# Kernel tuning notes

Hardware: AMD Instinct MI355X
Metric: run time of the kernel (lower is better)

Reference implementation:

```python
import jax, jax.numpy as jnp
import numpy as np

INPUT_SIZE = 1024  # enc_dim + dec_dim after concat
ENC_DIM = 512
DEC_DIM = 512
INNER_DIM = 512
VOCAB = 2048


def setup_inputs() -> dict:
    key = jax.random.key(0)
    k1, k2, k3, k4, k5, k6 = jax.random.split(key, 6)
    B, T, U = 4, 256, 128
    enc_state = jax.random.normal(k1, (B, T, ENC_DIM), dtype=jnp.float32)
    dec_state = jax.random.normal(k2, (B, U, DEC_DIM), dtype=jnp.float32)
    # forward_layer: Linear(input_size, inner_dim); stored as [in, out] for jax
    s1 = 1.0 / np.sqrt(INPUT_SIZE)
    W1 = jax.random.uniform(k3, (INPUT_SIZE, INNER_DIM), jnp.float32, -s1, s1)
    b1 = jax.random.uniform(k4, (INNER_DIM,), jnp.float32, -s1, s1)
    s2 = 1.0 / np.sqrt(INNER_DIM)
    W2 = jax.random.uniform(k5, (INNER_DIM, VOCAB), jnp.float32, -s2, s2)
    b2 = jax.random.uniform(k6, (VOCAB,), jnp.float32, -s2, s2)
    return {"enc_state": enc_state, "dec_state": dec_state,
            "W1": W1, "b1": b1, "W2": W2, "b2": b2}


def reference(enc_state, dec_state, W1, b1, W2, b2):
    # JointNet: concat(enc_repeat, dec_repeat) @ W1 + b1 -> tanh -> @ W2 + b2.
    # Since W1 acts on the concat axis, split it: concat @ W1 == enc @ W1_e + dec @ W1_d
    # (mathematically identical, avoids materializing the [B,T,U,2D] concat tensor).
    W1_enc = W1[:ENC_DIM]   # [D_enc, inner]
    W1_dec = W1[ENC_DIM:]   # [D_dec, inner]
    enc_proj = jnp.einsum('btd,dh->bth', enc_state, W1_enc)  # [B,T,H]
    dec_proj = jnp.einsum('bud,dh->buh', dec_state, W1_dec)  # [B,U,H]
    h = jnp.tanh(enc_proj[:, :, None, :] + dec_proj[:, None, :, :] + b1)  # [B,T,U,H]
    logits = jnp.einsum('btuh,hv->btuv', h, W2) + b2  # [B,T,U,V]
    return logits
```

## Files before the change

### kernel.cpp

```cpp
#include <hip/hip_runtime.h>
#include <hip/hip_bf16.h>


typedef __attribute__((ext_vector_type(4))) float f32x4;
typedef __attribute__((ext_vector_type(8))) __bf16 bf16x8;
typedef __attribute__((ext_vector_type(8))) unsigned short u16x8;

__device__ __forceinline__ float bf2f(unsigned short u) {
  unsigned int x = ((unsigned int)u) << 16;
  return __builtin_bit_cast(float, x);
}
__device__ __forceinline__ unsigned short f2bf(float f) {
  unsigned int x = __builtin_bit_cast(unsigned int, f);
  x += 0x7fff + ((x >> 16) & 1);
  return (unsigned short)(x >> 16);
}
__device__ __forceinline__ float tanh_fast(float x) {
  float e = __expf(2.0f * x);
  return 1.0f - 2.0f * __builtin_amdgcn_rcpf(e + 1.0f);
}

typedef __attribute__((address_space(3))) unsigned int lds_u32;
typedef const __attribute__((address_space(1))) unsigned int glb_u32;
__device__ __forceinline__ void gl16(const void* g, void* l) {
  __builtin_amdgcn_global_load_lds((glb_u32*)g, (lds_u32*)l, 16, 0, 0);
}

#define BAR __builtin_amdgcn_s_barrier()
#define LGKM0 asm volatile("s_waitcnt lgkmcnt(0)" ::: "memory")
#define VMCNT(n) asm volatile("s_waitcnt vmcnt(" #n ")" ::: "memory")
#define MEMPIN asm volatile("" ::: "memory")

__global__ __launch_bounds__(512) void proj8_kernel(
    const float* __restrict__ enc, const float* __restrict__ dec,
    const float* __restrict__ W1, const float* __restrict__ b1,
    float* __restrict__ enc_proj, unsigned short* __restrict__ decb) {
  __shared__ float xs[8][512];
  const int bid = blockIdx.x;
  const bool isenc = bid < 128;
  const int rows0 = (isenc ? bid : bid - 128) * 8;
  const float* src = (isenc ? enc : dec) + (size_t)rows0 * 512;
  const int tid = threadIdx.x;
#pragma unroll
  for (int j = 0; j < 2; ++j) {
    int v = j * 512 + tid;
    int row = v >> 7;
    int c4 = (v & 127) << 2;
    *(f32x4*)&xs[row][c4] = *(const f32x4*)&src[(size_t)row * 512 + c4];
  }
  __syncthreads();
  const int h = tid;
  const float* wp = W1 + (isenc ? 0 : (size_t)512 * 512) + h;
  float acc[8];
  float init = isenc ? 0.f : b1[h];
#pragma unroll
  for (int r = 0; r < 8; ++r) acc[r] = init;
#pragma unroll 4
  for (int k = 0; k < 512; ++k) {
    float wv = wp[(size_t)k * 512];
#pragma unroll
    for (int r = 0; r < 8; ++r) acc[r] = fmaf(xs[r][k], wv, acc[r]);
  }
  if (isenc) {
#pragma unroll
    for (int r = 0; r < 8; ++r) enc_proj[(size_t)(rows0 + r) * 512 + h] = acc[r];
  } else {
#pragma unroll
    for (int r = 0; r < 8; ++r) decb[(size_t)(rows0 + r) * 512 + h] = f2bf(acc[r]);
  }
}

__global__ __launch_bounds__(256) void w2t_kernel(const float* __restrict__ W2,
                                                  unsigned short* __restrict__ W2t) {
  __shared__ unsigned short tile[32][33];
  int bn = blockIdx.x;
  int bk = blockIdx.y;
  int tx = threadIdx.x & 31;
  int ty = threadIdx.x >> 5;
#pragma unroll
  for (int i = 0; i < 32; i += 8)
    tile[ty + i][tx] = f2bf(W2[(size_t)(bk * 32 + ty + i) * 2048 + bn * 32 + tx]);
  __syncthreads();
#pragma unroll
  for (int i = 0; i < 32; i += 8)
    W2t[(size_t)(bn * 32 + ty + i) * 512 + bk * 32 + tx] = tile[tx][ty + i];
}

__global__ __launch_bounds__(256) void h_kernel(
    const float* __restrict__ encp, const unsigned short* __restrict__ decb,
    unsigned short* __restrict__ Hout) {
  int gid = blockIdx.x * 256 + threadIdx.x;
  int m = gid >> 6;
  int hc = (gid & 63) << 3;
  int bt = m >> 7;
  int bu = ((m >> 15) << 7) | (m & 127);
  u16x8 dv = *(const u16x8*)(decb + (size_t)bu * 512 + hc);
  f32x4 e0 = *(const f32x4*)(encp + (size_t)bt * 512 + hc);
  f32x4 e1 = *(const f32x4*)(encp + (size_t)bt * 512 + hc + 4);
  u16x8 hv;
#pragma unroll
  for (int j = 0; j < 4; ++j) hv[j] = f2bf(tanh_fast(bf2f(dv[j]) + e0[j]));
#pragma unroll
  for (int j = 0; j < 4; ++j) hv[4 + j] = f2bf(tanh_fast(bf2f(dv[4 + j]) + e1[j]));
  *(u16x8*)(Hout + (size_t)m * 512 + hc) = hv;
}

__device__ __forceinline__ void stage_half(const char* src, char* dst_region,
                                           int half, int w, int lane) {
#pragma unroll
  for (int r = 0; r < 2; ++r) {
    int dbase = half * 16384 + r * 8192 + w * 1024;
    int d = dbase + lane * 16;
    int s = d ^ (((d >> 9) & 1) << 5);
    gl16(src + (size_t)(s >> 7) * 1024 + (s & 127), dst_region + dbase);
  }
}

__device__ __forceinline__ void load_a(const char* Ar, int a_base, int MH,
                                       bf16x8 (&afr)[4][2]) {
#pragma unroll
  for (int mi = 0; mi < 4; ++mi)
#pragma unroll
    for (int kk = 0; kk < 2; ++kk)
      afr[mi][kk] = *(const bf16x8*)(Ar + a_base + MH * 8192 + mi * 2048 + kk * 64);
}
__device__ __forceinline__ void load_b(const char* Br, int b_base, int NH,
                                       bf16x8 (&bh)[2][2]) {
#pragma unroll
  for (int ni = 0; ni < 2; ++ni)
#pragma unroll
    for (int kk = 0; kk < 2; ++kk)
      bh[ni][kk] = *(const bf16x8*)(Br + b_base + NH * 4096 + ni * 2048 + kk * 64);
}

template <int MH, int NH>
__device__ __forceinline__ void mfma_quad(bf16x8 (&afr)[4][2], bf16x8 (&bh)[2][2],
                                          f32x4 (&acc)[8][4]) {
  __builtin_amdgcn_s_setprio(1);
#pragma unroll
  for (int mi = 0; mi < 4; ++mi)
#pragma unroll
    for (int ni = 0; ni < 2; ++ni)
#pragma unroll
      for (int kk = 0; kk < 2; ++kk)
        acc[MH * 4 + mi][NH * 2 + ni] = __builtin_amdgcn_mfma_f32_16x16x32_bf16(
            afr[mi][kk], bh[ni][kk], acc[MH * 4 + mi][NH * 2 + ni], 0, 0, 0);
  __builtin_amdgcn_s_setprio(0);
}

__global__ __launch_bounds__(512, 2) void gemm8_kernel(
    const unsigned short* __restrict__ H,
    const unsigned short* __restrict__ W2t,
    const float* __restrict__ b2,
    float* __restrict__ out) {
  __shared__ __align__(1024) char smem[131072];
  char* A0 = smem;
  char* B0 = smem + 32768;
  char* A1 = smem + 65536;
  char* B1 = smem + 98304;

  const int bid = blockIdx.x;
  const int wg = (bid & 7) * 512 + (bid >> 3);
  const int my = wg >> 3;
  const int ny = wg & 7;

  const int tid = threadIdx.x;
  const int lane = tid & 63;
  const int w = tid >> 6;
  const int wm = w >> 2;
  const int wn = w & 3;
  const int fr = lane & 15;
  const int fq = lane >> 4;
  const int xr = (fr & 4) ? 32 : 0;

  const char* ha = (const char*)(H + (size_t)my * 256 * 512);
  const char* wb = (const char*)(W2t + (size_t)ny * 256 * 512);

  const int a_base = (wm * 128 + fr) * 128 + ((fq * 16) ^ xr);
  const int b_base = (wn * 64 + fr) * 128 + ((fq * 16) ^ xr);

  f32x4 acc[8][4];
#pragma unroll
  for (int i = 0; i < 8; ++i)
#pragma unroll
    for (int j = 0; j < 4; ++j) acc[i][j] = (f32x4){0.f, 0.f, 0.f, 0.f};
  bf16x8 afr[4][2];
  bf16x8 bfr[2][2][2];

  stage_half(ha, A0, 0, w, lane);        stage_half(ha, A0, 1, w, lane);
  stage_half(wb, B0, 0, w, lane);        stage_half(wb, B0, 1, w, lane);
  stage_half(ha + 128, A1, 0, w, lane);  stage_half(ha + 128, A1, 1, w, lane);
  stage_half(wb + 128, B1, 0, w, lane);  stage_half(wb + 128, B1, 1, w, lane);
  VMCNT(0);
  BAR; MEMPIN;

  for (int i = 0; i < 4; ++i) {
    const int t = 2 * i;
    const char* sA1 = ha + (size_t)(t + 1) * 128;
    const char* sA2 = ha + (size_t)(t + 2) * 128;
    const char* sB2 = wb + (size_t)(t + 2) * 128;
    const char* sB3 = wb + (size_t)(t + 3) * 128;
    const bool si = (i >= 1);
    const bool so = (i <= 2);

    load_a(A0, a_base, 0, afr);
    load_b(B0, b_base, 0, bfr[0]);
    if (si) stage_half(sA1, A1, 0, w, lane);
    BAR; LGKM0;
    mfma_quad<0, 0>(afr, bfr[0], acc);
    BAR; MEMPIN;

    load_b(B0, b_base, 1, bfr[1]);
    if (si) stage_half(sA1, A1, 1, w, lane);
    BAR; LGKM0;
    mfma_quad<0, 1>(afr, bfr[1], acc);
    BAR; MEMPIN;

    load_a(A0, a_base, 1, afr);
    if (so) stage_half(sB2, B0, 0, w, lane);
    BAR; LGKM0;
    mfma_quad<1, 0>(afr, bfr[0], acc);
    BAR; MEMPIN;

    if (so) {
      stage_half(sB2, B0, 1, w, lane);
      stage_half(sA2, A0, 0, w, lane);
      stage_half(sA2, A0, 1, w, lane);
    }
    BAR; LGKM0;
    mfma_quad<1, 1>(afr, bfr[1], acc);
    if (i < 3) { VMCNT(8); } else { VMCNT(0); }
    BAR; MEMPIN;

    load_a(A1, a_base, 0, afr);
    load_b(B1, b_base, 0, bfr[0]);
    BAR; LGKM0;
    mfma_quad<0, 0>(afr, bfr[0], acc);
    BAR; MEMPIN;

    load_b(B1, b_base, 1, bfr[1]);
    BAR; LGKM0;
    mfma_quad<0, 1>(afr, bfr[1], acc);
    BAR; MEMPIN;

    load_a(A1, a_base, 1, afr);
    if (so) stage_half(sB3, B1, 0, w, lane);
    BAR; LGKM0;
    mfma_quad<1, 0>(afr, bfr[0], acc);
    BAR; MEMPIN;

    if (so) stage_half(sB3, B1, 1, w, lane);
    BAR; LGKM0;
    mfma_quad<1, 1>(afr, bfr[1], acc);
    if (i < 3) { VMCNT(4); } else { VMCNT(0); }
    BAR; MEMPIN;
  }

  float* lslice = (float*)(smem + w * 4352);
  const size_t orow0 = (size_t)my * 256 + wm * 128;
  const int ncol0 = ny * 256 + wn * 64;
  float bv[4];
#pragma unroll
  for (int ni4 = 0; ni4 < 4; ++ni4) bv[ni4] = b2[ncol0 + ni4 * 16 + fr];

  const int rrow = lane >> 4;
  const int rcol = (lane & 15) * 4;
#pragma unroll
  for (int mi8 = 0; mi8 < 8; ++mi8) {
#pragma unroll
    for (int ni4 = 0; ni4 < 4; ++ni4)
#pragma unroll
      for (int r = 0; r < 4; ++r)
        lslice[(fq * 4 + r) * 68 + ni4 * 16 + fr] = acc[mi8][ni4][r] + bv[ni4];
#pragma unroll
    for (int j = 0; j < 4; ++j) {
      int row = j * 4 + rrow;
      f32x4 v = *(const f32x4*)&lslice[row * 68 + rcol];
      __builtin_nontemporal_store(
          v, (f32x4*)&out[(orow0 + mi8 * 16 + row) * 2048 + ncol0 + rcol]);
    }
  }
}

extern "C" void kernel_launch(void* const* d_in, const int* in_sizes, int n_in,
                              void* d_out, int out_size, void* d_ws, size_t ws_size,
                              hipStream_t stream) {
  const float* enc = (const float*)d_in[0];
  const float* dec = (const float*)d_in[1];
  const float* W1  = (const float*)d_in[2];
  const float* b1  = (const float*)d_in[3];
  const float* W2  = (const float*)d_in[4];
  const float* b2  = (const float*)d_in[5];
  float* out = (float*)d_out;

  char* ws = (char*)d_ws;
  float* enc_proj = (float*)ws;
  unsigned short* decb = (unsigned short*)(ws + (2u << 20));
  unsigned short* W2t  = (unsigned short*)(ws + (2u << 20) + (512u << 10));
  unsigned short* Hbuf = (unsigned short*)(ws + (8u << 20));

  proj8_kernel<<<192, 512, 0, stream>>>(enc, dec, W1, b1, enc_proj, decb);
  w2t_kernel<<<dim3(64, 16), 256, 0, stream>>>(W2, W2t);
  h_kernel<<<32768, 256, 0, stream>>>(enc_proj, decb, Hbuf);
  gemm8_kernel<<<4096, 512, 0, stream>>>(Hbuf, W2t, b2, out);
}
```

Before: 427.0 us.

## Replace 256x256 GEMM tile with 256x128 tile and 3-stage K=32 pipeline

The main logits GEMM drops its 256x256 output tile, 8-wave 2x4 layout and 128KB double buffer. It now uses a 256x128 tile with a 4x2 wave layout and K steps of 32 through a 3-slot, 72KB LDS ring with XOR swizzle. This allows up to 4 blocks per CU and uses a simpler one-barrier-per-step schedule, aiming for higher occupancy and better latency hiding. In exchange, W2 tiles are reused less, H is re-read twice as often, and barriers are more frequent.

Result: faster. 406.1 us (-4.9%).

```diff
diff --git a/kernel.cpp b/kernel.cpp
--- a/kernel.cpp
+++ b/kernel.cpp
@@ -105,181 +105,114 @@
   *(u16x8*)(Hout + (size_t)m * 512 + hc) = hv;
 }
 
-__device__ __forceinline__ void stage_half(const char* src, char* dst_region,
-                                           int half, int w, int lane) {
-#pragma unroll
-  for (int r = 0; r < 2; ++r) {
-    int dbase = half * 16384 + r * 8192 + w * 1024;
-    int d = dbase + lane * 16;
-    int s = d ^ (((d >> 9) & 1) << 5);
-    gl16(src + (size_t)(s >> 7) * 1024 + (s & 127), dst_region + dbase);
-  }
-}
-
-__device__ __forceinline__ void load_a(const char* Ar, int a_base, int MH,
-                                       bf16x8 (&afr)[4][2]) {
-#pragma unroll
-  for (int mi = 0; mi < 4; ++mi)
-#pragma unroll
-    for (int kk = 0; kk < 2; ++kk)
-      afr[mi][kk] = *(const bf16x8*)(Ar + a_base + MH * 8192 + mi * 2048 + kk * 64);
-}
-__device__ __forceinline__ void load_b(const char* Br, int b_base, int NH,
-                                       bf16x8 (&bh)[2][2]) {
-#pragma unroll
-  for (int ni = 0; ni < 2; ++ni)
-#pragma unroll
-    for (int kk = 0; kk < 2; ++kk)
-      bh[ni][kk] = *(const bf16x8*)(Br + b_base + NH * 4096 + ni * 2048 + kk * 64);
-}
-
-template <int MH, int NH>
-__device__ __forceinline__ void mfma_quad(bf16x8 (&afr)[4][2], bf16x8 (&bh)[2][2],
-                                          f32x4 (&acc)[8][4]) {
-  __builtin_amdgcn_s_setprio(1);
-#pragma unroll
-  for (int mi = 0; mi < 4; ++mi)
-#pragma unroll
-    for (int ni = 0; ni < 2; ++ni)
-#pragma unroll
-      for (int kk = 0; kk < 2; ++kk)
-        acc[MH * 4 + mi][NH * 2 + ni] = __builtin_amdgcn_mfma_f32_16x16x32_bf16(
-            afr[mi][kk], bh[ni][kk], acc[MH * 4 + mi][NH * 2 + ni], 0, 0, 0);
-  __builtin_amdgcn_s_setprio(0);
-}
-
-__global__ __launch_bounds__(512, 2) void gemm8_kernel(
+
+__global__ __launch_bounds__(512, 4) void gemm32_kernel(
     const unsigned short* __restrict__ H,
     const unsigned short* __restrict__ W2t,
     const float* __restrict__ b2,
     float* __restrict__ out) {
-  __shared__ __align__(1024) char smem[131072];
-  char* A0 = smem;
-  char* B0 = smem + 32768;
-  char* A1 = smem + 65536;
-  char* B1 = smem + 98304;
+  __shared__ __align__(1024) char smem[73728];
 
   const int bid = blockIdx.x;
-  const int wg = (bid & 7) * 512 + (bid >> 3);
-  const int my = wg >> 3;
-  const int ny = wg & 7;
+  const int wg = (bid & 7) * 1024 + (bid >> 3);
+  const int my = wg >> 4;
+  const int ny = wg & 15;
 
   const int tid = threadIdx.x;
   const int lane = tid & 63;
   const int w = tid >> 6;
-  const int wm = w >> 2;
-  const int wn = w & 3;
+  const int wm = w >> 1;
+  const int wn = w & 1;
   const int fr = lane & 15;
   const int fq = lane >> 4;
-  const int xr = (fr & 4) ? 32 : 0;
 
   const char* ha = (const char*)(H + (size_t)my * 256 * 512);
-  const char* wb = (const char*)(W2t + (size_t)ny * 256 * 512);
-
-  const int a_base = (wm * 128 + fr) * 128 + ((fq * 16) ^ xr);
-  const int b_base = (wn * 64 + fr) * 128 + ((fq * 16) ^ xr);
-
-  f32x4 acc[8][4];
-#pragma unroll
-  for (int i = 0; i < 8; ++i)
+  const char* wb = (const char*)(W2t + (size_t)ny * 128 * 512);
+
+  size_t srcA[2], srcB;
+#pragma unroll
+  for (int p = 0; p < 2; ++p) {
+    int d = p * 8192 + w * 1024 + lane * 16;
+    int r = d >> 6;
+    int c = (d >> 4) & 3;
+    srcA[p] = (size_t)r * 1024 + (size_t)((c ^ (r & 3)) << 4);
+  }
+  {
+    int d = w * 1024 + lane * 16;
+    int r = d >> 6;
+    int c = (d >> 4) & 3;
+    srcB = (size_t)r * 1024 + (size_t)((c ^ (r & 3)) << 4);
+  }
+
+  const int swz = (fq ^ (fr & 3)) << 4;
+  const int ldsA = (wm * 64 + fr) * 64 + swz;
+  const int ldsB = 16384 + (wn * 64 + fr) * 64 + swz;
+
+  f32x4 acc[4][4];
+#pragma unroll
+  for (int i = 0; i < 4; ++i)
 #pragma unroll
     for (int j = 0; j < 4; ++j) acc[i][j] = (f32x4){0.f, 0.f, 0.f, 0.f};
-  bf16x8 afr[4][2];
-  bf16x8 bfr[2][2][2];
-
-  stage_half(ha, A0, 0, w, lane);        stage_half(ha, A0, 1, w, lane);
-  stage_half(wb, B0, 0, w, lane);        stage_half(wb, B0, 1, w, lane);
-  stage_half(ha + 128, A1, 0, w, lane);  stage_half(ha + 128, A1, 1, w, lane);
-  stage_half(wb + 128, B1, 0, w, lane);  stage_half(wb + 128, B1, 1, w, lane);
-  VMCNT(0);
+
+#define STAGE(tt, slot)                                         \
+  do {                                                          \
+    char* sl = smem + (slot)*24576;                             \
+    gl16(ha + srcA[0] + (tt)*64, sl + w * 1024);                \
+    gl16(ha + srcA[1] + (tt)*64, sl + 8192 + w * 1024);         \
+    gl16(wb + srcB + (tt)*64, sl + 16384 + w * 1024);           \
+  } while (0)
+
+  STAGE(0, 0);
+  STAGE(1, 1);
+
+#pragma unroll
+  for (int t = 0; t < 16; ++t) {
+    if (t < 15) { VMCNT(3); } else { VMCNT(0); }
+    BAR; MEMPIN;
+    const char* As = smem + (t % 3) * 24576;
+    bf16x8 a4[4], b4[4];
+#pragma unroll
+    for (int mi = 0; mi < 4; ++mi) a4[mi] = *(const bf16x8*)(As + ldsA + mi * 1024);
+#pragma unroll
+    for (int ni = 0; ni < 4; ++ni) b4[ni] = *(const bf16x8*)(As + ldsB + ni * 1024);
+    if (t + 2 < 16) STAGE(t + 2, (t + 2) % 3);
+    LGKM0;
+    __builtin_amdgcn_s_setprio(1);
+#pragma unroll
+    for (int mi = 0; mi < 4; ++mi)
+#pragma unroll
+      for (int ni = 0; ni < 4; ++ni)
+        acc[mi][ni] = __builtin_amdgcn_mfma_f32_16x16x32_bf16(
+            a4[mi], b4[ni], acc[mi][ni], 0, 0, 0);
+    __builtin_amdgcn_s_setprio(0);
+  }
   BAR; MEMPIN;
 
-  for (int i = 0; i < 4; ++i) {
-    const int t = 2 * i;
-    const char* sA1 = ha + (size_t)(t + 1) * 128;
-    const char* sA2 = ha + (size_t)(t + 2) * 128;
-    const char* sB2 = wb + (size_t)(t + 2) * 128;
-    const char* sB3 = wb + (size_t)(t + 3) * 128;
-    const bool si = (i >= 1);
-    const bool so = (i <= 2);
-
-    load_a(A0, a_base, 0, afr);
-    load_b(B0, b_base, 0, bfr[0]);
-    if (si) stage_half(sA1, A1, 0, w, lane);
-    BAR; LGKM0;
-    mfma_quad<0, 0>(afr, bfr[0], acc);
-    BAR; MEMPIN;
-
-    load_b(B0, b_base, 1, bfr[1]);
-    if (si) stage_half(sA1, A1, 1, w, lane);
-    BAR; LGKM0;
-    mfma_quad<0, 1>(afr, bfr[1], acc);
-    BAR; MEMPIN;
-
-    load_a(A0, a_base, 1, afr);
-    if (so) stage_half(sB2, B0, 0, w, lane);
-    BAR; LGKM0;
-    mfma_quad<1, 0>(afr, bfr[0], acc);
-    BAR; MEMPIN;
-
-    if (so) {
-      stage_half(sB2, B0, 1, w, lane);
-      stage_half(sA2, A0, 0, w, lane);
-      stage_half(sA2, A0, 1, w, lane);
-    }
-    BAR; LGKM0;
-    mfma_quad<1, 1>(afr, bfr[1], acc);
-    if (i < 3) { VMCNT(8); } else { VMCNT(0); }
-    BAR; MEMPIN;
-
-    load_a(A1, a_base, 0, afr);
-    load_b(B1, b_base, 0, bfr[0]);
-    BAR; LGKM0;
-    mfma_quad<0, 0>(afr, bfr[0], acc);
-    BAR; MEMPIN;
-
-    load_b(B1, b_base, 1, bfr[1]);
-    BAR; LGKM0;
-    mfma_quad<0, 1>(afr, bfr[1], acc);
-    BAR; MEMPIN;
-
-    load_a(A1, a_base, 1, afr);
-    if (so) stage_half(sB3, B1, 0, w, lane);
-    BAR; LGKM0;
-    mfma_quad<1, 0>(afr, bfr[0], acc);
-    BAR; MEMPIN;
-
-    if (so) stage_half(sB3, B1, 1, w, lane);
-    BAR; LGKM0;
-    mfma_quad<1, 1>(afr, bfr[1], acc);
-    if (i < 3) { VMCNT(4); } else { VMCNT(0); }
-    BAR; MEMPIN;
-  }
-
   float* lslice = (float*)(smem + w * 4352);
-  const size_t orow0 = (size_t)my * 256 + wm * 128;
-  const int ncol0 = ny * 256 + wn * 64;
+  const size_t orow0 = (size_t)my * 256 + wm * 64;
+  const int ncol0 = ny * 128 + wn * 64;
   float bv[4];
 #pragma unroll
-  for (int ni4 = 0; ni4 < 4; ++ni4) bv[ni4] = b2[ncol0 + ni4 * 16 + fr];
+  for (int ni = 0; ni < 4; ++ni) bv[ni] = b2[ncol0 + ni * 16 + fr];
 
   const int rrow = lane >> 4;
   const int rcol = (lane & 15) * 4;
 #pragma unroll
-  for (int mi8 = 0; mi8 < 8; ++mi8) {
-#pragma unroll
-    for (int ni4 = 0; ni4 < 4; ++ni4)
+  for (int mi = 0; mi < 4; ++mi) {
+#pragma unroll
+    for (int ni = 0; ni < 4; ++ni)
 #pragma unroll
       for (int r = 0; r < 4; ++r)
-        lslice[(fq * 4 + r) * 68 + ni4 * 16 + fr] = acc[mi8][ni4][r] + bv[ni4];
+        lslice[(fq * 4 + r) * 68 + ni * 16 + fr] = acc[mi][ni][r] + bv[ni];
 #pragma unroll
     for (int j = 0; j < 4; ++j) {
       int row = j * 4 + rrow;
       f32x4 v = *(const f32x4*)&lslice[row * 68 + rcol];
       __builtin_nontemporal_store(
-          v, (f32x4*)&out[(orow0 + mi8 * 16 + row) * 2048 + ncol0 + rcol]);
+          v, (f32x4*)&out[(orow0 + mi * 16 + row) * 2048 + ncol0 + rcol]);
     }
   }
+#undef STAGE
 }
 
 extern "C" void kernel_launch(void* const* d_in, const int* in_sizes, int n_in,
@@ -302,5 +235,5 @@
   proj8_kernel<<<192, 512, 0, stream>>>(enc, dec, W1, b1, enc_proj, decb);
   w2t_kernel<<<dim3(64, 16), 256, 0, stream>>>(W2, W2t);
   h_kernel<<<32768, 256, 0, stream>>>(enc_proj, decb, Hbuf);
-  gemm8_kernel<<<4096, 512, 0, stream>>>(Hbuf, W2t, b2, out);
-}
+  gemm32_kernel<<<8192, 512, 0, stream>>>(Hbuf, W2t, b2, out);
+}
```
